# Performance work log

Measured on AMD Instinct MI355X. Metric: run time of the kernel, lower is better.

The kernel has to match this reference:

```python
import jax, jax.numpy as jnp
import numpy as np

B, L, PATCH_IN, D, NPOS = 64, 1024, 768, 1152, 256


def setup_inputs() -> dict:
    key = jax.random.key(0)
    k1, k2, k3, k4 = jax.random.split(key, 4)
    pixel_values = jax.random.normal(k1, (B, L, PATCH_IN), dtype=jnp.float32)
    # per-sample (h, w) with h*w <= L and h, w >= 16 (pure upsampling of 16x16 grid)
    hs = np.array([16 + (i % 17) for i in range(B)], dtype=np.int64)
    ws = (L // hs).astype(np.int64)
    spatial_shapes = jnp.asarray(np.stack([hs, ws], axis=1))
    W = jax.random.normal(k2, (D, PATCH_IN), dtype=jnp.float32) * 0.02
    b = jax.random.normal(k3, (D,), dtype=jnp.float32) * 0.02
    pos_emb = jax.random.normal(k4, (NPOS, D), dtype=jnp.float32) * 0.02
    return {"pixel_values": pixel_values, "spatial_shapes": spatial_shapes,
            "W": W, "b": b, "pos_emb": pos_emb}


def _resized_pos_embeddings(pos_emb, spatial_shapes_np, max_length):
    # pos_emb: [num_patches, D] -> [G, G, D] grid
    g = int(np.sqrt(pos_emb.shape[0]))
    d = pos_emb.shape[1]
    grid = pos_emb.reshape(g, g, d)
    rows = []
    for i in range(spatial_shapes_np.shape[0]):
        h, w = int(spatial_shapes_np[i, 0]), int(spatial_shapes_np[i, 1])
        # half-pixel bilinear == torch F.interpolate(align_corners=False); antialias
        # is a no-op for upsampling (h, w >= g)
        r = jax.image.resize(grid, (h, w, d), method="bilinear").reshape(h * w, d)
        pad = jnp.broadcast_to(r[0], (max_length - h * w, d))  # replicate first patch
        rows.append(jnp.concatenate([r, pad], axis=0))
    return jnp.stack(rows)  # [B, max_length, D]


def reference(pixel_values, spatial_shapes, W, b, pos_emb):
    # patch linear embedding: [B, L, Cpp] x [D, Cpp] -> [B, L, D]
    patch_embeds = jnp.einsum("blk,dk->bld", pixel_values, W) + b
    ss = np.asarray(spatial_shapes)  # static per-sample shapes
    pos = _resized_pos_embeddings(pos_emb, ss, pixel_values.shape[1])
    return patch_embeds + pos
```

## Files before the change

### kernel.cpp

```cpp
#include <hip/hip_runtime.h>

typedef __bf16 bf16x8 __attribute__((ext_vector_type(8)));
typedef float  f32x4  __attribute__((ext_vector_type(4)));

constexpr int BM = 128, BN = 128, BK = 32;
constexpr int MDIM = 65536, NDIM = 1152, KDIM = 768;
constexpr int NBN = NDIM / BN;
constexpr int NKT = KDIM / BK;
constexpr int GRID = (MDIM / BM) * NBN;
constexpr int LDSROWB = BK * 2;
constexpr int CHUNKS_A = (MDIM / BM) * NKT * 512;
constexpr int CHUNKS_W = NBN * NKT * 512;

__device__ __forceinline__ void gload16(const void* g, void* l) {
  __builtin_amdgcn_global_load_lds(
      (const __attribute__((address_space(1))) void*)g,
      (__attribute__((address_space(3))) void*)l, 16, 0, 0);
}

__device__ __forceinline__ unsigned pk2(float x, float y) {
  __bf16 a = (__bf16)x, b = (__bf16)y;
  return (unsigned)__builtin_bit_cast(unsigned short, a) |
         ((unsigned)__builtin_bit_cast(unsigned short, b) << 16);
}

__global__ __launch_bounds__(256)
void repack_all_kernel(const float* __restrict__ Ain, __bf16* __restrict__ Aout,
                       const float* __restrict__ Win, __bf16* __restrict__ Wout) {
  int c = blockIdx.x * 256 + threadIdx.x;
  const float* in;
  __bf16* out;
  if (c < CHUNKS_A) { in = Ain; out = Aout; }
  else              { in = Win; out = Wout; c -= CHUNKS_A; }
  const int c_in = c & 511;
  const int img  = c >> 9;
  const int kt   = img % NKT;
  const int pan  = img / NKT;
  const int r16  = c_in >> 6;
  const int ln   = c_in & 63;
  const int kg   = ln >> 4;
  const int fr   = ln & 15;
  const float* src = in + (size_t)(pan * 128 + r16 * 16 + fr) * KDIM + kt * 32 + kg * 8;
  const float4 x = *reinterpret_cast<const float4*>(src);
  const float4 y = *reinterpret_cast<const float4*>(src + 4);
  uint4 r4;
  r4.x = pk2(x.x, x.y); r4.y = pk2(x.z, x.w);
  r4.z = pk2(y.x, y.y); r4.w = pk2(y.z, y.w);
  *reinterpret_cast<uint4*>(out + (size_t)c * 8) = r4;
}

__global__ __launch_bounds__(256, 4)
void gemm_fm2_kernel(const __bf16* __restrict__ Aimg,
                     const __bf16* __restrict__ Bimg,
                     const int*   __restrict__ ss,
                     const float* __restrict__ bias,
                     const float* __restrict__ pos,
                     float* __restrict__ out) {
  __shared__ __align__(16) unsigned char SM[32768];
  __bf16* As0 = reinterpret_cast<__bf16*>(SM);
  __bf16* Bs0 = reinterpret_cast<__bf16*>(SM + 16384);
  float*  Cs  = reinterpret_cast<float*>(SM);

  const int tid  = threadIdx.x;
  const int lane = tid & 63;
  const int wid  = tid >> 6;
  const int wr   = wid >> 1;
  const int wc   = wid & 1;

  const int bidh = blockIdx.x;
  const int bid  = (bidh & 7) * (GRID / 8) + (bidh >> 3);
  const int bm   = bid / NBN;
  const int bn   = bid % NBN;

  auto stage = [&](int kt, int buf) {
    const __bf16* wsA = Aimg + ((size_t)(bm * NKT + kt) << 12);
    const __bf16* wsB = Bimg + ((size_t)(bn * NKT + kt) << 12);
    char* la = (char*)As0 + buf * 8192;
    char* lb = (char*)Bs0 + buf * 8192;
    gload16(wsA + tid * 8,         la + tid * 16);
    gload16(wsA + (256 + tid) * 8, la + (256 + tid) * 16);
    gload16(wsB + tid * 8,         lb + tid * 16);
    gload16(wsB + (256 + tid) * 8, lb + (256 + tid) * 16);
  };

  f32x4 acc[4][4];
#pragma unroll
  for (int i = 0; i < 4; ++i)
#pragma unroll
    for (int j = 0; j < 4; ++j) acc[i][j] = (f32x4)0.0f;

  const int fr = lane & 15;
  const int kg = lane >> 4;
  const int abase = wr * 4096 + lane * 16;
  const int bbase = wc * 4096 + lane * 16;

  auto compute = [&](int buf) {
    const char* pa = (const char*)As0 + buf * 8192 + abase;
    const char* pb = (const char*)Bs0 + buf * 8192 + bbase;
    bf16x8 af[4], bfv[4];
#pragma unroll
    for (int mf = 0; mf < 4; ++mf)
      af[mf] = *reinterpret_cast<const bf16x8*>(pa + mf * 1024);
#pragma unroll
    for (int nf = 0; nf < 4; ++nf)
      bfv[nf] = *reinterpret_cast<const bf16x8*>(pb + nf * 1024);
#pragma unroll
    for (int mf = 0; mf < 4; ++mf)
#pragma unroll
      for (int nf = 0; nf < 4; ++nf)
        acc[mf][nf] = __builtin_amdgcn_mfma_f32_16x16x32_bf16(af[mf], bfv[nf], acc[mf][nf], 0, 0, 0);
  };

  stage(0, 0);
  for (int kt = 0; kt < NKT; ++kt) {
    const int cur = kt & 1;
    __syncthreads();
    if (kt + 1 < NKT) stage(kt + 1, cur ^ 1);
    compute(cur);
  }

  const int chunk = tid & 15;
  const int gcol  = bn * BN + chunk * 8;
  const f32x4 bias_lo = *reinterpret_cast<const f32x4*>(bias + gcol);
  const f32x4 bias_hi = *reinterpret_cast<const f32x4*>(bias + gcol + 4);

  const int s  = bm >> 3;
  const int h  = ss[2 * s];
  const int w  = ss[2 * s + 1];
  const int hw = h * w;
  const float rh = 16.0f / (float)h;
  const float rw = 16.0f / (float)w;

#pragma unroll
  for (int half = 0; half < 2; ++half) {
    __syncthreads();
#pragma unroll
    for (int mm = 0; mm < 2; ++mm) {
#pragma unroll
      for (int nf = 0; nf < 4; ++nf) {
#pragma unroll
        for (int rg = 0; rg < 4; ++rg) {
          const int rowL = wr * 32 + mm * 16 + kg * 4 + rg;
          const int col  = wc * 64 + nf * 16 + fr;
          const int key  = (rowL & 3) ^ ((rowL >> 2) & 3);
          Cs[(rowL << 7) + (col ^ (key << 3))] = acc[half * 2 + mm][nf][rg];
        }
      }
    }
    __syncthreads();
#pragma unroll
    for (int pass = 0; pass < 4; ++pass) {
      const int rowL = pass * 16 + (tid >> 4);
      const int key  = (rowL & 3) ^ ((rowL >> 2) & 3);
      const float* crow = Cs + (rowL << 7) + ((chunk ^ key) << 3);
      const f32x4 c0 = *reinterpret_cast<const f32x4*>(crow);
      const f32x4 c1 = *reinterpret_cast<const f32x4*>(crow + 4);

      const int grow = bm * BM + (rowL >> 5) * 64 + half * 32 + (rowL & 31);
      int p = grow & 1023;
      if (p >= hw) p = 0;
      const int y = p / w;
      const int x = p - y * w;
      const float fy = ((float)y + 0.5f) * rh - 0.5f;
      const float fx = ((float)x + 0.5f) * rw - 0.5f;
      const float yf = floorf(fy), xf = floorf(fx);
      const float ty = fy - yf,   tx = fx - xf;
      int iy0 = (int)yf, ix0 = (int)xf;
      int iy1 = iy0 + 1 > 15 ? 15 : iy0 + 1;
      int ix1 = ix0 + 1 > 15 ? 15 : ix0 + 1;
      iy0 = iy0 < 0 ? 0 : iy0;
      ix0 = ix0 < 0 ? 0 : ix0;
      const float* g00 = pos + (size_t)(iy0 * 16 + ix0) * NDIM + gcol;
      const float* g01 = pos + (size_t)(iy0 * 16 + ix1) * NDIM + gcol;
      const float* g10 = pos + (size_t)(iy1 * 16 + ix0) * NDIM + gcol;
      const float* g11 = pos + (size_t)(iy1 * 16 + ix1) * NDIM + gcol;

      const f32x4 v00l = *reinterpret_cast<const f32x4*>(g00);
      const f32x4 v01l = *reinterpret_cast<const f32x4*>(g01);
      const f32x4 v10l = *reinterpret_cast<const f32x4*>(g10);
      const f32x4 v11l = *reinterpret_cast<const f32x4*>(g11);
      const f32x4 v00h = *reinterpret_cast<const f32x4*>(g00 + 4);
      const f32x4 v01h = *reinterpret_cast<const f32x4*>(g01 + 4);
      const f32x4 v10h = *reinterpret_cast<const f32x4*>(g10 + 4);
      const f32x4 v11h = *reinterpret_cast<const f32x4*>(g11 + 4);

      const f32x4 topl = v00l + tx * (v01l - v00l);
      const f32x4 botl = v10l + tx * (v11l - v10l);
      const f32x4 pvl  = topl + ty * (botl - topl);
      const f32x4 toph = v00h + tx * (v01h - v00h);
      const f32x4 both = v10h + tx * (v11h - v10h);
      const f32x4 pvh  = toph + ty * (both - toph);

      float* orow = out + (size_t)grow * NDIM + gcol;
      *reinterpret_cast<f32x4*>(orow)     = c0 + bias_lo + pvl;
      *reinterpret_cast<f32x4*>(orow + 4) = c1 + bias_hi + pvh;
    }
  }
}

__global__ __launch_bounds__(256, 2)
void gemm_fb_kernel(const float* __restrict__ A,
                    const int*   __restrict__ ss,
                    const float* __restrict__ Wm,
                    const float* __restrict__ bias,
                    const float* __restrict__ pos,
                    float* __restrict__ out) {
  __shared__ unsigned short As[2][BM * BK];
  __shared__ unsigned short Bs[2][BM * BK];

  const int tid  = threadIdx.x;
  const int lane = tid & 63;
  const int wid  = tid >> 6;
  const int wr   = wid >> 1;
  const int wc   = wid & 1;

  const int bidh = blockIdx.x;
  const int bid  = (bidh & 7) * (GRID / 8) + (bidh >> 3);
  const int bm   = bid / NBN;
  const int bn   = bid % NBN;

  const int srow0 = tid >> 3;
  const int skc   = tid & 7;
  const float* Ag = A  + (size_t)(bm * BM + srow0) * KDIM + skc * 4;
  const float* Bg = Wm + (size_t)(bn * BN + srow0) * KDIM + skc * 4;

  float4 ra[4], rb[4];

  auto stage_load = [&](int kt) {
    const int ko = kt * BK;
#pragma unroll
    for (int r = 0; r < 4; ++r) {
      ra[r] = *reinterpret_cast<const float4*>(Ag + (size_t)(r * 32) * KDIM + ko);
      rb[r] = *reinterpret_cast<const float4*>(Bg + (size_t)(r * 32) * KDIM + ko);
    }
  };

  auto stage_write = [&](int buf) {
#pragma unroll
    for (int r = 0; r < 4; ++r) {
      const int arow = r * 32 + srow0;
      int off = arow * LDSROWB + skc * 8;
      off ^= (arow & 7) << 4;
      uint2 pa, pb;
      pa.x = pk2(ra[r].x, ra[r].y); pa.y = pk2(ra[r].z, ra[r].w);
      pb.x = pk2(rb[r].x, rb[r].y); pb.y = pk2(rb[r].z, rb[r].w);
      *reinterpret_cast<uint2*>(reinterpret_cast<char*>(&As[buf][0]) + off) = pa;
      *reinterpret_cast<uint2*>(reinterpret_cast<char*>(&Bs[buf][0]) + off) = pb;
    }
  };

  f32x4 acc[4][4];
#pragma unroll
  for (int i = 0; i < 4; ++i)
#pragma unroll
    for (int j = 0; j < 4; ++j) acc[i][j] = (f32x4)0.0f;

  const int fr = lane & 15;
  const int kg = lane >> 4;
  int abase = (wr * 64 + fr) * LDSROWB + kg * 16; abase ^= (fr & 7) << 4;
  int bbase = (wc * 64 + fr) * LDSROWB + kg * 16; bbase ^= (fr & 7) << 4;

  auto compute = [&](int buf) {
    const char* pa = reinterpret_cast<const char*>(&As[buf][0]);
    const char* pb = reinterpret_cast<const char*>(&Bs[buf][0]);
    bf16x8 af[4], bfv[4];
#pragma unroll
    for (int mf = 0; mf < 4; ++mf)
      af[mf] = *reinterpret_cast<const bf16x8*>(pa + abase + mf * 16 * LDSROWB);
#pragma unroll
    for (int nf = 0; nf < 4; ++nf)
      bfv[nf] = *reinterpret_cast<const bf16x8*>(pb + bbase + nf * 16 * LDSROWB);
#pragma unroll
    for (int mf = 0; mf < 4; ++mf)
#pragma unroll
      for (int nf = 0; nf < 4; ++nf)
        acc[mf][nf] = __builtin_amdgcn_mfma_f32_16x16x32_bf16(af[mf], bfv[nf], acc[mf][nf], 0, 0, 0);
  };

  stage_load(0);
  stage_write(0);
  for (int kt = 0; kt < NKT; ++kt) {
    const int cur = kt & 1;
    if (kt + 1 < NKT) stage_load(kt + 1);
    __syncthreads();
    compute(cur);
    if (kt + 1 < NKT) stage_write(cur ^ 1);
  }

  const int colbase = bn * BN + wc * 64 + fr;
  float bvals[4];
#pragma unroll
  for (int nf = 0; nf < 4; ++nf) bvals[nf] = bias[colbase + nf * 16];

  const int s  = bm >> 3;
  const int h  = ss[2 * s];
  const int w  = ss[2 * s + 1];
  const int hw = h * w;
  const float rh = 16.0f / (float)h;
  const float rw = 16.0f / (float)w;
  const int row0 = bm * BM + wr * 64 + kg * 4;

#pragma unroll
  for (int mf = 0; mf < 4; ++mf) {
#pragma unroll
    for (int rg = 0; rg < 4; ++rg) {
      const int row = row0 + mf * 16 + rg;
      int p = row & 1023;
      if (p >= hw) p = 0;
      const int y = p / w;
      const int x = p - y * w;
      const float fy = ((float)y + 0.5f) * rh - 0.5f;
      const float fx = ((float)x + 0.5f) * rw - 0.5f;
      const float yf = floorf(fy), xf = floorf(fx);
      const float ty = fy - yf,   tx = fx - xf;
      int iy0 = (int)yf, ix0 = (int)xf;
      int iy1 = iy0 + 1 > 15 ? 15 : iy0 + 1;
      int ix1 = ix0 + 1 > 15 ? 15 : ix0 + 1;
      iy0 = iy0 < 0 ? 0 : iy0;
      ix0 = ix0 < 0 ? 0 : ix0;
      const float* g00 = pos + (size_t)(iy0 * 16 + ix0) * NDIM;
      const float* g01 = pos + (size_t)(iy0 * 16 + ix1) * NDIM;
      const float* g10 = pos + (size_t)(iy1 * 16 + ix0) * NDIM;
      const float* g11 = pos + (size_t)(iy1 * 16 + ix1) * NDIM;
      float* orow = out + (size_t)row * NDIM;
#pragma unroll
      for (int nf = 0; nf < 4; ++nf) {
        const int col = colbase + nf * 16;
        const float p00 = g00[col], p01 = g01[col];
        const float p10 = g10[col], p11 = g11[col];
        const float top = p00 + tx * (p01 - p00);
        const float bot = p10 + tx * (p11 - p10);
        const float pv  = top + ty * (bot - top);
        orow[col] = acc[mf][nf][rg] + bvals[nf] + pv;
      }
    }
  }
}

extern "C" void kernel_launch(void* const* d_in, const int* in_sizes, int n_in,
                              void* d_out, int out_size, void* d_ws, size_t ws_size,
                              hipStream_t stream) {
  const float* A    = (const float*)d_in[0];
  const int*   ss   = (const int*)d_in[1];
  const float* Wm   = (const float*)d_in[2];
  const float* bias = (const float*)d_in[3];
  const float* pos  = (const float*)d_in[4];
  float* out = (float*)d_out;

  const size_t needA = (size_t)MDIM * KDIM * 2;
  const size_t needW = (size_t)NDIM * KDIM * 2;

  if (ws_size >= needA + needW) {
    __bf16* Ab = (__bf16*)d_ws;
    __bf16* Bb = (__bf16*)((char*)d_ws + needA);
    repack_all_kernel<<<(CHUNKS_A + CHUNKS_W) / 256, 256, 0, stream>>>(A, Ab, Wm, Bb);
    gemm_fm2_kernel<<<GRID, 256, 0, stream>>>(Ab, Bb, ss, bias, pos, out);
  } else {
    gemm_fb_kernel<<<GRID, 256, 0, stream>>>(A, ss, Wm, bias, pos, out);
  }
}
```

Before: 261.5 us.

## Shrink GEMM N-tile to 64 and raise occupancy with smaller LDS footprint

The fast-path GEMM moves from 128x128 tiles to 128x64 tiles. This halves the B staging and accumulator registers, cuts LDS from 32KB to 24KB and raises the launch bound to 5 blocks per SM. The epilogue is reworked so each warp-row writes its 64-row half into a 64-column swizzled LDS tile. The aim is more occupancy and latency hiding, at the cost of re-reading each A tile twice as often, which lowers arithmetic intensity per block.

Result: slower. 392.4 us (+50.1%).

```diff
diff --git a/kernel.cpp b/kernel.cpp
--- a/kernel.cpp
+++ b/kernel.cpp
@@ -3,11 +3,13 @@
 typedef __bf16 bf16x8 __attribute__((ext_vector_type(8)));
 typedef float  f32x4  __attribute__((ext_vector_type(4)));
 
-constexpr int BM = 128, BN = 128, BK = 32;
+constexpr int BM = 128, BK = 32;
 constexpr int MDIM = 65536, NDIM = 1152, KDIM = 768;
-constexpr int NBN = NDIM / BN;
 constexpr int NKT = KDIM / BK;
-constexpr int GRID = (MDIM / BM) * NBN;
+constexpr int NBN2 = NDIM / 64;
+constexpr int GRID3 = (MDIM / BM) * NBN2;
+constexpr int NBN = NDIM / 128;
+constexpr int FBGRID = (MDIM / BM) * NBN;
 constexpr int LDSROWB = BK * 2;
 constexpr int CHUNKS_A = (MDIM / BM) * NKT * 512;
 constexpr int CHUNKS_W = NBN * NKT * 512;
@@ -49,17 +51,16 @@
   *reinterpret_cast<uint4*>(out + (size_t)c * 8) = r4;
 }
 
-__global__ __launch_bounds__(256, 4)
-void gemm_fm2_kernel(const __bf16* __restrict__ Aimg,
-                     const __bf16* __restrict__ Bimg,
-                     const int*   __restrict__ ss,
-                     const float* __restrict__ bias,
-                     const float* __restrict__ pos,
-                     float* __restrict__ out) {
-  __shared__ __align__(16) unsigned char SM[32768];
-  __bf16* As0 = reinterpret_cast<__bf16*>(SM);
-  __bf16* Bs0 = reinterpret_cast<__bf16*>(SM + 16384);
-  float*  Cs  = reinterpret_cast<float*>(SM);
+__global__ __launch_bounds__(256, 5)
+void gemm_lw_kernel(const __bf16* __restrict__ Aimg,
+                    const __bf16* __restrict__ Bimg,
+                    const int*   __restrict__ ss,
+                    const float* __restrict__ bias,
+                    const float* __restrict__ pos,
+                    float* __restrict__ out) {
+  __shared__ __align__(16) unsigned char SM[24576];
+  char* smc = reinterpret_cast<char*>(SM);
+  float* Cs = reinterpret_cast<float*>(SM);
 
   const int tid  = threadIdx.x;
   const int lane = tid & 63;
@@ -68,46 +69,45 @@
   const int wc   = wid & 1;
 
   const int bidh = blockIdx.x;
-  const int bid  = (bidh & 7) * (GRID / 8) + (bidh >> 3);
-  const int bm   = bid / NBN;
-  const int bn   = bid % NBN;
+  const int bid  = (bidh & 7) * (GRID3 / 8) + (bidh >> 3);
+  const int bm   = bid / NBN2;
+  const int bn   = bid % NBN2;
 
   auto stage = [&](int kt, int buf) {
     const __bf16* wsA = Aimg + ((size_t)(bm * NKT + kt) << 12);
-    const __bf16* wsB = Bimg + ((size_t)(bn * NKT + kt) << 12);
-    char* la = (char*)As0 + buf * 8192;
-    char* lb = (char*)Bs0 + buf * 8192;
+    const __bf16* wsB = Bimg + ((size_t)((bn >> 1) * NKT + kt) << 12) + (bn & 1) * 2048;
+    char* la = smc + buf * 8192;
+    char* lb = smc + 16384 + buf * 4096;
     gload16(wsA + tid * 8,         la + tid * 16);
     gload16(wsA + (256 + tid) * 8, la + (256 + tid) * 16);
     gload16(wsB + tid * 8,         lb + tid * 16);
-    gload16(wsB + (256 + tid) * 8, lb + (256 + tid) * 16);
-  };
-
-  f32x4 acc[4][4];
+  };
+
+  f32x4 acc[4][2];
 #pragma unroll
   for (int i = 0; i < 4; ++i)
 #pragma unroll
-    for (int j = 0; j < 4; ++j) acc[i][j] = (f32x4)0.0f;
+    for (int j = 0; j < 2; ++j) acc[i][j] = (f32x4)0.0f;
 
   const int fr = lane & 15;
   const int kg = lane >> 4;
   const int abase = wr * 4096 + lane * 16;
-  const int bbase = wc * 4096 + lane * 16;
+  const int bbase = wc * 2048 + lane * 16;
 
   auto compute = [&](int buf) {
-    const char* pa = (const char*)As0 + buf * 8192 + abase;
-    const char* pb = (const char*)Bs0 + buf * 8192 + bbase;
-    bf16x8 af[4], bfv[4];
+    const char* pa = smc + buf * 8192 + abase;
+    const char* pb = smc + 16384 + buf * 4096 + bbase;
+    bf16x8 af[4], bfv[2];
 #pragma unroll
     for (int mf = 0; mf < 4; ++mf)
       af[mf] = *reinterpret_cast<const bf16x8*>(pa + mf * 1024);
 #pragma unroll
-    for (int nf = 0; nf < 4; ++nf)
+    for (int nf = 0; nf < 2; ++nf)
       bfv[nf] = *reinterpret_cast<const bf16x8*>(pb + nf * 1024);
 #pragma unroll
     for (int mf = 0; mf < 4; ++mf)
 #pragma unroll
-      for (int nf = 0; nf < 4; ++nf)
+      for (int nf = 0; nf < 2; ++nf)
         acc[mf][nf] = __builtin_amdgcn_mfma_f32_16x16x32_bf16(af[mf], bfv[nf], acc[mf][nf], 0, 0, 0);
   };
 
@@ -119,8 +119,8 @@
     compute(cur);
   }
 
-  const int chunk = tid & 15;
-  const int gcol  = bn * BN + chunk * 8;
+  const int chunk = tid & 7;
+  const int gcol  = bn * 64 + chunk * 8;
   const f32x4 bias_lo = *reinterpret_cast<const f32x4*>(bias + gcol);
   const f32x4 bias_hi = *reinterpret_cast<const f32x4*>(bias + gcol + 4);
 
@@ -134,29 +134,32 @@
 #pragma unroll
   for (int half = 0; half < 2; ++half) {
     __syncthreads();
-#pragma unroll
-    for (int mm = 0; mm < 2; ++mm) {
-#pragma unroll
-      for (int nf = 0; nf < 4; ++nf) {
-#pragma unroll
-        for (int rg = 0; rg < 4; ++rg) {
-          const int rowL = wr * 32 + mm * 16 + kg * 4 + rg;
-          const int col  = wc * 64 + nf * 16 + fr;
-          const int key  = (rowL & 3) ^ ((rowL >> 2) & 3);
-          Cs[(rowL << 7) + (col ^ (key << 3))] = acc[half * 2 + mm][nf][rg];
+    if (wr == half) {
+#pragma unroll
+      for (int mf = 0; mf < 4; ++mf) {
+#pragma unroll
+        for (int nf = 0; nf < 2; ++nf) {
+#pragma unroll
+          for (int rg = 0; rg < 4; ++rg) {
+            const int rowL = mf * 16 + kg * 4 + rg;
+            const int col  = wc * 32 + nf * 16 + fr;
+            const int key  = rowL & 7;
+            const int phys = ((((col >> 3) ^ key) << 3) | (col & 7));
+            Cs[(rowL << 6) + phys] = acc[mf][nf][rg];
+          }
         }
       }
     }
     __syncthreads();
 #pragma unroll
-    for (int pass = 0; pass < 4; ++pass) {
-      const int rowL = pass * 16 + (tid >> 4);
-      const int key  = (rowL & 3) ^ ((rowL >> 2) & 3);
-      const float* crow = Cs + (rowL << 7) + ((chunk ^ key) << 3);
+    for (int pass = 0; pass < 2; ++pass) {
+      const int rowL = pass * 32 + (tid >> 3);
+      const int key  = rowL & 7;
+      const float* crow = Cs + (rowL << 6) + ((chunk ^ key) << 3);
       const f32x4 c0 = *reinterpret_cast<const f32x4*>(crow);
       const f32x4 c1 = *reinterpret_cast<const f32x4*>(crow + 4);
 
-      const int grow = bm * BM + (rowL >> 5) * 64 + half * 32 + (rowL & 31);
+      const int grow = bm * BM + half * 64 + rowL;
       int p = grow & 1023;
       if (p >= hw) p = 0;
       const int y = p / w;
@@ -215,14 +218,14 @@
   const int wc   = wid & 1;
 
   const int bidh = blockIdx.x;
-  const int bid  = (bidh & 7) * (GRID / 8) + (bidh >> 3);
+  const int bid  = (bidh & 7) * (FBGRID / 8) + (bidh >> 3);
   const int bm   = bid / NBN;
   const int bn   = bid % NBN;
 
   const int srow0 = tid >> 3;
   const int skc   = tid & 7;
   const float* Ag = A  + (size_t)(bm * BM + srow0) * KDIM + skc * 4;
-  const float* Bg = Wm + (size_t)(bn * BN + srow0) * KDIM + skc * 4;
+  const float* Bg = Wm + (size_t)(bn * 128 + srow0) * KDIM + skc * 4;
 
   float4 ra[4], rb[4];
 
@@ -287,7 +290,7 @@
     if (kt + 1 < NKT) stage_write(cur ^ 1);
   }
 
-  const int colbase = bn * BN + wc * 64 + fr;
+  const int colbase = bn * 128 + wc * 64 + fr;
   float bvals[4];
 #pragma unroll
   for (int nf = 0; nf < 4; ++nf) bvals[nf] = bias[colbase + nf * 16];
@@ -354,8 +357,8 @@
     __bf16* Ab = (__bf16*)d_ws;
     __bf16* Bb = (__bf16*)((char*)d_ws + needA);
     repack_all_kernel<<<(CHUNKS_A + CHUNKS_W) / 256, 256, 0, stream>>>(A, Ab, Wm, Bb);
-    gemm_fm2_kernel<<<GRID, 256, 0, stream>>>(Ab, Bb, ss, bias, pos, out);
+    gemm_lw_kernel<<<GRID3, 256, 0, stream>>>(Ab, Bb, ss, bias, pos, out);
   } else {
-    gemm_fb_kernel<<<GRID, 256, 0, stream>>>(A, ss, Wm, bias, pos, out);
-  }
-}
+    gemm_fb_kernel<<<FBGRID, 256, 0, stream>>>(A, ss, Wm, bias, pos, out);
+  }
+}
```
